# Performance work log

Measured on AMD Instinct MI355X. Metric: run time of the kernel, lower is better.

The kernel has to match this reference:

```python
import jax, jax.numpy as jnp
import numpy as np

NUM_HEADS = 4
LN_EPS = 1e-5


def setup_inputs() -> dict:
    key = jax.random.key(0)
    ks = jax.random.split(key, 5)
    C = 256
    x = jax.random.normal(ks[0], (2, C, 64, 64), dtype=jnp.float32)
    in_proj_w = jax.random.normal(ks[1], (3 * C, C), dtype=jnp.float32) * (1.0 / np.sqrt(C))
    in_proj_b = jax.random.normal(ks[2], (3 * C,), dtype=jnp.float32) * 0.02
    out_w = jax.random.normal(ks[3], (C, C), dtype=jnp.float32) * (1.0 / np.sqrt(C))
    out_b = jax.random.normal(ks[4], (C,), dtype=jnp.float32) * 0.02
    ln_g = jnp.ones((C,), dtype=jnp.float32)
    ln_b = jnp.zeros((C,), dtype=jnp.float32)
    return {"x": x, "in_proj_w": in_proj_w, "in_proj_b": in_proj_b,
            "out_w": out_w, "out_b": out_b, "ln_g": ln_g, "ln_b": ln_b}


def reference(x, in_proj_w, in_proj_b, out_w, out_b, ln_g, ln_b):
    b, c, H, W = x.shape
    S = H * W  # 4096 == max_tokens -> no pooling, no interpolation
    hd = c // NUM_HEADS
    t = x.reshape(b, c, S).transpose(0, 2, 1)  # (b, S, c)
    # fused QKV projection (in_proj_weight is [3c, c], rows = q,k,v blocks)
    qkv = t @ in_proj_w.T + in_proj_b  # (b, S, 3c)
    q, k, v = jnp.split(qkv, 3, axis=-1)
    def to_heads(a):
        return a.reshape(b, S, NUM_HEADS, hd).transpose(0, 2, 1, 3)  # (b, h, S, d)
    q = to_heads(q) * (1.0 / np.sqrt(hd))
    k = to_heads(k)
    v = to_heads(v)
    scores = jnp.einsum('bhqd,bhkd->bhqk', q, k)      # (b, h, S, S)
    probs = jax.nn.softmax(scores, axis=-1)
    attn = jnp.einsum('bhqk,bhkd->bhqd', probs, v)    # (b, h, S, d)
    attn = attn.transpose(0, 2, 1, 3).reshape(b, S, c)
    out = attn @ out_w.T + out_b                      # output projection
    # LayerNorm over channel dim
    mu = jnp.mean(out, axis=-1, keepdims=True)
    var = jnp.mean(jnp.square(out - mu), axis=-1, keepdims=True)
    out = (out - mu) * jax.lax.rsqrt(var + LN_EPS) * ln_g + ln_b
    return out.transpose(0, 2, 1).reshape(b, c, H, W)
```

## Files before the change

### kernel.cpp

```cpp
#include <hip/hip_runtime.h>
#include <cstddef>

#define S_TOK 4096
#define CDIM 256
#define NHEADS 4
#define HDIM 64
#define LSK 72
#define LDA 36
#define LDY 264
#define LOG2E 1.44269504f

typedef __attribute__((ext_vector_type(8))) short short8;
typedef __attribute__((ext_vector_type(4))) float floatx4;

__device__ inline unsigned short f2bf(float f) {
  union { float f; unsigned u; } v;
  v.f = f;
  unsigned r = v.u + 0x7fff + ((v.u >> 16) & 1);
  return (unsigned short)(r >> 16);
}
__device__ inline float bf2f(unsigned short u) {
  union { unsigned u; float f; } v;
  v.u = ((unsigned)u) << 16;
  return v.f;
}
__device__ inline unsigned pack_bf16(float a, float b) {
#if __has_builtin(__builtin_amdgcn_cvt_pk_bf16_f32)
  typedef __bf16 bf16x2 __attribute__((ext_vector_type(2)));
  union { bf16x2 v; unsigned u; } r;
  r.v = __builtin_amdgcn_cvt_pk_bf16_f32(a, b);
  return r.u;
#else
  unsigned r;
  asm("v_cvt_pk_bf16_f32 %0, %1, %2" : "=v"(r) : "v"(a), "v"(b));
  return r;
#endif
}

__device__ inline void pl32swap(unsigned& a, unsigned& b) {
  asm("v_permlane32_swap_b32 %0, %1" : "+v"(a), "+v"(b));
}
__device__ inline void pl16swap(unsigned& a, unsigned& b) {
  asm("v_permlane16_swap_b32 %0, %1" : "+v"(a), "+v"(b));
}

__global__ __launch_bounds__(256) void qkv_gemm_kernel(
    const float* __restrict__ x, const float* __restrict__ ipw,
    const float* __restrict__ ipb, unsigned short* __restrict__ q16,
    unsigned short* __restrict__ k16, unsigned short* __restrict__ vt16) {
  __shared__ __align__(16) unsigned short As[64 * LDA];
  __shared__ __align__(16) unsigned short Bs[3][64 * LDA];
  const int tid = threadIdx.x;
  const int wave = tid >> 6, lane = tid & 63;
  const int quad = lane >> 4, l16 = lane & 15;
  const int n0 = blockIdx.x * 64;
  const int tok0 = blockIdx.y * 64;
  const int b = blockIdx.z;

  const int c_l = tid >> 3, t8 = tid & 7;
  const float* gx = x + (((size_t)(b * CDIM + c_l)) << 12) + tok0 + t8 * 8;
  unsigned short* wa = &As[(t8 * 8) * LDA + c_l];

  const int rr = tid >> 2, c4 = tid & 3;
  const float* gw0 = ipw + ((size_t)(n0 + rr)) * CDIM + c4 * 8;
  unsigned short* wb0 = &Bs[0][rr * LDA + c4 * 8];

  floatx4 acc[3][4];
#pragma unroll
  for (int s = 0; s < 3; ++s)
#pragma unroll
    for (int nt = 0; nt < 4; ++nt) acc[s][nt] = (floatx4){0.f, 0.f, 0.f, 0.f};

  float4 a0 = *(const float4*)(gx);
  float4 a1 = *(const float4*)(gx + 4);
  float4 bp[3][2];
#pragma unroll
  for (int s = 0; s < 3; ++s) {
    bp[s][0] = *(const float4*)(gw0 + (size_t)s * 256 * CDIM);
    bp[s][1] = *(const float4*)(gw0 + (size_t)s * 256 * CDIM + 4);
  }

  for (int ks = 0; ks < 8; ++ks) {
    __syncthreads();
    {
      unsigned p;
      p = pack_bf16(a0.x, a0.y);
      wa[0 * LDA] = (unsigned short)p; wa[1 * LDA] = (unsigned short)(p >> 16);
      p = pack_bf16(a0.z, a0.w);
      wa[2 * LDA] = (unsigned short)p; wa[3 * LDA] = (unsigned short)(p >> 16);
      p = pack_bf16(a1.x, a1.y);
      wa[4 * LDA] = (unsigned short)p; wa[5 * LDA] = (unsigned short)(p >> 16);
      p = pack_bf16(a1.z, a1.w);
      wa[6 * LDA] = (unsigned short)p; wa[7 * LDA] = (unsigned short)(p >> 16);
    }
#pragma unroll
    for (int s = 0; s < 3; ++s) {
      uint2 u0, u1;
      u0.x = pack_bf16(bp[s][0].x, bp[s][0].y);
      u0.y = pack_bf16(bp[s][0].z, bp[s][0].w);
      u1.x = pack_bf16(bp[s][1].x, bp[s][1].y);
      u1.y = pack_bf16(bp[s][1].z, bp[s][1].w);
      unsigned short* w = wb0 + s * 64 * LDA;
      *(uint2*)w = u0;
      *(uint2*)(w + 4) = u1;
    }
    __syncthreads();
    if (ks < 7) {
      const float* gxn = gx + ((size_t)((ks + 1) * 32) << 12);
      a0 = *(const float4*)(gxn);
      a1 = *(const float4*)(gxn + 4);
#pragma unroll
      for (int s = 0; s < 3; ++s) {
        const float* g = gw0 + (size_t)s * 256 * CDIM + (ks + 1) * 32;
        bp[s][0] = *(const float4*)(g);
        bp[s][1] = *(const float4*)(g + 4);
      }
    }
    short8 af = *(const short8*)&As[(wave * 16 + l16) * LDA + quad * 8];
#pragma unroll
    for (int s = 0; s < 3; ++s)
#pragma unroll
      for (int nt = 0; nt < 4; ++nt) {
        short8 bf = *(const short8*)&Bs[s][(nt * 16 + l16) * LDA + quad * 8];
        acc[s][nt] = __builtin_amdgcn_mfma_f32_16x16x32_bf16(af, bf, acc[s][nt], 0, 0, 0);
      }
  }

  const float qsc = 0.125f * LOG2E;
#pragma unroll
  for (int nt = 0; nt < 4; ++nt) {
    int cb = n0 + nt * 16 + l16;
    int h = cb >> 6, dh = cb & 63;
    float bq = ipb[cb], bk = ipb[256 + cb], bv = ipb[512 + cb];
    size_t base = ((size_t)(b * NHEADS + h)) * S_TOK;
#pragma unroll
    for (int r = 0; r < 4; ++r) {
      int tok = tok0 + wave * 16 + quad * 4 + r;
      q16[(base + tok) * HDIM + dh] = f2bf((acc[0][nt][r] + bq) * qsc);
      k16[(base + tok) * HDIM + dh] = f2bf(acc[1][nt][r] + bk);
    }
    int tokv = tok0 + wave * 16 + quad * 4;
    uint2 u;
    u.x = pack_bf16(acc[2][nt][0] + bv, acc[2][nt][1] + bv);
    u.y = pack_bf16(acc[2][nt][2] + bv, acc[2][nt][3] + bv);
    *(uint2*)&vt16[(base * 0 + ((size_t)(b * NHEADS + h) * HDIM + dh)) * S_TOK + tokv] = u;
  }
}

__global__ __launch_bounds__(256) void attn_kernel(
    const unsigned short* __restrict__ q16,
    const unsigned short* __restrict__ k16,
    const unsigned short* __restrict__ vt16,
    unsigned short* __restrict__ op, float* __restrict__ lp) {
  __shared__ __align__(16) unsigned short Ks[2][64 * LSK];
  __shared__ __align__(16) unsigned short Vt[2][64 * LSK];

  const int tid = threadIdx.x;
  const int wave = tid >> 6;
  const int lane = tid & 63;
  const int quad = lane >> 4;
  const int l16 = lane & 15;
  const int bh = blockIdx.y;
  const int q0 = blockIdx.x * 256;
  const int split = blockIdx.z;
  const int kt0 = split * 16;

  short8 qf[4][2];
#pragma unroll
  for (int mt = 0; mt < 4; ++mt) {
    const unsigned short* qg =
        q16 + ((size_t)bh * S_TOK + q0 + wave * 64 + mt * 16 + l16) * HDIM + quad * 8;
    qf[mt][0] = *(const short8*)(qg);
    qf[mt][1] = *(const short8*)(qg + 32);
  }

  const int sr = tid >> 3, scc = tid & 7;
  const unsigned short* kg = k16 + ((size_t)bh * S_TOK + sr) * HDIM + scc * 8;
  const unsigned short* vg = vt16 + ((size_t)bh * HDIM + sr) * S_TOK + scc * 8;

  floatx4 O[4][4];
  float lsum[4] = {0.f, 0.f, 0.f, 0.f};
#pragma unroll
  for (int mt = 0; mt < 4; ++mt)
#pragma unroll
    for (int nt = 0; nt < 4; ++nt) O[mt][nt] = (floatx4){0.f, 0.f, 0.f, 0.f};

  uint4 k0r = *(const uint4*)(kg + (size_t)kt0 * 64 * HDIM);
  uint4 k1r = *(const uint4*)(kg + (size_t)kt0 * 64 * HDIM + 32 * HDIM);
  uint4 v0r = *(const uint4*)(vg + kt0 * 64);
  uint4 v1r = *(const uint4*)(vg + kt0 * 64 + (size_t)32 * S_TOK);
  {
    unsigned short* kw = &Ks[0][sr * LSK + scc * 8];
    unsigned short* vw = &Vt[0][sr * LSK + scc * 8];
    *(uint4*)kw = k0r;
    *(uint4*)(kw + 32 * LSK) = k1r;
    *(uint4*)vw = v0r;
    *(uint4*)(vw + 32 * LSK) = v1r;
  }
  __syncthreads();

  for (int t = 0; t < 16; ++t) {
    const int cur = t & 1;
    if (t < 15) {
      const unsigned short* kgn = kg + (size_t)(kt0 + t + 1) * 64 * HDIM;
      const unsigned short* vgn = vg + (kt0 + t + 1) * 64;
      k0r = *(const uint4*)(kgn);
      k1r = *(const uint4*)(kgn + 32 * HDIM);
      v0r = *(const uint4*)(vgn);
      v1r = *(const uint4*)(vgn + (size_t)32 * S_TOK);
    }
    const unsigned short* Kb = Ks[cur];
    const unsigned short* Vb = Vt[cur];

#pragma unroll
    for (int c = 0; c < 2; ++c) {
      short8 kfA0 = *(const short8*)(&Kb[((c * 2) * 16 + l16) * LSK + quad * 8]);
      short8 kfA1 = *(const short8*)(&Kb[((c * 2) * 16 + l16) * LSK + 32 + quad * 8]);
      short8 kfB0 = *(const short8*)(&Kb[((c * 2 + 1) * 16 + l16) * LSK + quad * 8]);
      short8 kfB1 = *(const short8*)(&Kb[((c * 2 + 1) * 16 + l16) * LSK + 32 + quad * 8]);
      short8 vf[4];
#pragma unroll
      for (int nt = 0; nt < 4; ++nt)
        vf[nt] = *(const short8*)(&Vb[(nt * 16 + l16) * LSK + c * 32 + quad * 8]);
#pragma unroll
      for (int mt = 0; mt < 4; ++mt) {
        floatx4 cA = (floatx4){0.f, 0.f, 0.f, 0.f};
        cA = __builtin_amdgcn_mfma_f32_16x16x32_bf16(kfA0, qf[mt][0], cA, 0, 0, 0);
        cA = __builtin_amdgcn_mfma_f32_16x16x32_bf16(kfA1, qf[mt][1], cA, 0, 0, 0);
        floatx4 cB = (floatx4){0.f, 0.f, 0.f, 0.f};
        cB = __builtin_amdgcn_mfma_f32_16x16x32_bf16(kfB0, qf[mt][0], cB, 0, 0, 0);
        cB = __builtin_amdgcn_mfma_f32_16x16x32_bf16(kfB1, qf[mt][1], cB, 0, 0, 0);
        float a0 = __builtin_amdgcn_exp2f(cA[0]);
        float a1 = __builtin_amdgcn_exp2f(cA[1]);
        float a2 = __builtin_amdgcn_exp2f(cA[2]);
        float a3 = __builtin_amdgcn_exp2f(cA[3]);
        float b0 = __builtin_amdgcn_exp2f(cB[0]);
        float b1 = __builtin_amdgcn_exp2f(cB[1]);
        float b2 = __builtin_amdgcn_exp2f(cB[2]);
        float b3 = __builtin_amdgcn_exp2f(cB[3]);
        lsum[mt] += ((a0 + a1) + (a2 + a3)) + ((b0 + b1) + (b2 + b3));
        unsigned A0 = pack_bf16(a0, a1), B0 = pack_bf16(a2, a3);
        unsigned A1 = pack_bf16(b0, b1), B1 = pack_bf16(b2, b3);
        pl32swap(A0, A1); pl16swap(A0, A1);
        pl32swap(B0, B1); pl16swap(B0, B1);
        union { uint4 u; short8 s; } pf;
        pf.u.x = A0; pf.u.y = B0; pf.u.z = A1; pf.u.w = B1;
#pragma unroll
        for (int nt = 0; nt < 4; ++nt)
          O[mt][nt] = __builtin_amdgcn_mfma_f32_16x16x32_bf16(pf.s, vf[nt], O[mt][nt], 0, 0, 0);
      }
    }

    if (t < 15) {
      unsigned short* kw = &Ks[cur ^ 1][sr * LSK + scc * 8];
      unsigned short* vw = &Vt[cur ^ 1][sr * LSK + scc * 8];
      *(uint4*)kw = k0r;
      *(uint4*)(kw + 32 * LSK) = k1r;
      *(uint4*)vw = v0r;
      *(uint4*)(vw + 32 * LSK) = v1r;
      __syncthreads();
    }
  }

  const int b = bh >> 2, h = bh & 3;
  unsigned short* op_s = op + (size_t)split * 2097152;
  float* lp_s = lp + (size_t)split * 32768;
#pragma unroll
  for (int mt = 0; mt < 4; ++mt) {
    float ls = lsum[mt];
    ls += __shfl_xor(ls, 16);
    ls += __shfl_xor(ls, 32);
    if (quad == 0)
      lp_s[bh * S_TOK + q0 + wave * 64 + mt * 16 + l16] = ls;
#pragma unroll
    for (int r = 0; r < 4; ++r) {
      int row = q0 + wave * 64 + mt * 16 + quad * 4 + r;
#pragma unroll
      for (int nt = 0; nt < 4; ++nt)
        op_s[((size_t)(b * S_TOK + row)) * CDIM + h * HDIM + nt * 16 + l16] =
            f2bf(O[mt][nt][r]);
    }
  }
}

__device__ inline uint2 merge4(const unsigned short* op, size_t off, float rinv) {
  float s0 = 0.f, s1 = 0.f, s2 = 0.f, s3 = 0.f;
#pragma unroll
  for (int sp = 0; sp < 4; ++sp) {
    uint2 u = *(const uint2*)(op + (size_t)sp * 2097152 + off);
    s0 += bf2f((unsigned short)(u.x & 0xffff));
    s1 += bf2f((unsigned short)(u.x >> 16));
    s2 += bf2f((unsigned short)(u.y & 0xffff));
    s3 += bf2f((unsigned short)(u.y >> 16));
  }
  uint2 r;
  r.x = pack_bf16(s0 * rinv, s1 * rinv);
  r.y = pack_bf16(s2 * rinv, s3 * rinv);
  return r;
}

__global__ __launch_bounds__(256) void out_ln_gemm_kernel(
    const unsigned short* __restrict__ op, const float* __restrict__ lp,
    const float* __restrict__ ow, const float* __restrict__ obias,
    const float* __restrict__ lng, const float* __restrict__ lnb,
    float* __restrict__ out) {
  __shared__ __align__(16) unsigned short As[32 * LDA];
  __shared__ __align__(16) unsigned short Bs[256 * LDA];
  __shared__ __align__(16) float ys[32 * LDY];
  __shared__ float rsum[128];
  const int tid = threadIdx.x;
  const int wave = tid >> 6, lane = tid & 63;
  const int quad = lane >> 4, l16 = lane & 15;
  const int tok0 = blockIdx.x * 32;

  if (tid < 128) {
    int t = tid >> 2, h = tid & 3;
    int bb = tok0 >> 12;
    int idx = (bb * 4 + h) * 4096 + (tok0 & 4095) + t;
    rsum[tid] =
        1.0f / (lp[idx] + lp[32768 + idx] + lp[65536 + idx] + lp[98304 + idx]);
  }
  __syncthreads();

  const int ar = tid >> 3, ac = tid & 7;
  const size_t abase = (size_t)(tok0 + ar) * CDIM + ac * 4;
  unsigned short* wAp = &As[ar * LDA + ac * 4];
  const int rr = tid >> 2, c4 = tid & 3;
  const float* gB = ow + (size_t)rr * CDIM + c4 * 8;
  unsigned short* wBp = &Bs[rr * LDA + c4 * 8];

  floatx4 acc[2][4];
#pragma unroll
  for (int mt = 0; mt < 2; ++mt)
#pragma unroll
    for (int nt = 0; nt < 4; ++nt) acc[mt][nt] = (floatx4){0.f, 0.f, 0.f, 0.f};

  uint2 ap = merge4(op, abase, rsum[(ar << 2) + (ac >> 4)]);
  float4 bpf[4][2];
#pragma unroll
  for (int i = 0; i < 4; ++i) {
    bpf[i][0] = *(const float4*)(gB + (size_t)i * 64 * CDIM);
    bpf[i][1] = *(const float4*)(gB + (size_t)i * 64 * CDIM + 4);
  }

  for (int ks = 0; ks < 8; ++ks) {
    __syncthreads();
    *(uint2*)wAp = ap;
#pragma unroll
    for (int i = 0; i < 4; ++i) {
      uint2 u0, u1;
      u0.x = pack_bf16(bpf[i][0].x, bpf[i][0].y);
      u0.y = pack_bf16(bpf[i][0].z, bpf[i][0].w);
      u1.x = pack_bf16(bpf[i][1].x, bpf[i][1].y);
      u1.y = pack_bf16(bpf[i][1].z, bpf[i][1].w);
      unsigned short* w = wBp + i * 64 * LDA;
      *(uint2*)w = u0;
      *(uint2*)(w + 4) = u1;
    }
    __syncthreads();
    if (ks < 7) {
      int off = (ks + 1) * 32;
      int ch = off + ac * 4;
      ap = merge4(op, abase + off, rsum[(ar << 2) + (ch >> 6)]);
#pragma unroll
      for (int i = 0; i < 4; ++i) {
        bpf[i][0] = *(const float4*)(gB + (size_t)i * 64 * CDIM + off);
        bpf[i][1] = *(const float4*)(gB + (size_t)i * 64 * CDIM + off + 4);
      }
    }
    short8 af[2], bf[4];
#pragma unroll
    for (int mt = 0; mt < 2; ++mt)
      af[mt] = *(const short8*)&As[(mt * 16 + l16) * LDA + quad * 8];
#pragma unroll
    for (int nt = 0; nt < 4; ++nt)
      bf[nt] = *(const short8*)&Bs[(wave * 64 + nt * 16 + l16) * LDA + quad * 8];
#pragma unroll
    for (int mt = 0; mt < 2; ++mt)
#pragma unroll
      for (int nt = 0; nt < 4; ++nt)
        acc[mt][nt] = __builtin_amdgcn_mfma_f32_16x16x32_bf16(af[mt], bf[nt], acc[mt][nt], 0, 0, 0);
  }

#pragma unroll
  for (int mt = 0; mt < 2; ++mt)
#pragma unroll
    for (int nt = 0; nt < 4; ++nt) {
      int c = wave * 64 + nt * 16 + l16;
      float bo = obias[c];
#pragma unroll
      for (int r = 0; r < 4; ++r)
        ys[(mt * 16 + quad * 4 + r) * LDY + c] = acc[mt][nt][r] + bo;
    }
  __syncthreads();

  const int gtok = tid >> 3, l8 = tid & 7;
  float sum = 0.f, ssq = 0.f;
#pragma unroll
  for (int i = 0; i < 32; ++i) {
    float v = ys[gtok * LDY + i * 8 + l8];
    sum += v;
    ssq += v * v;
  }
  sum += __shfl_xor(sum, 1); ssq += __shfl_xor(ssq, 1);
  sum += __shfl_xor(sum, 2); ssq += __shfl_xor(ssq, 2);
  sum += __shfl_xor(sum, 4); ssq += __shfl_xor(ssq, 4);
  float mu = sum * (1.f / 256.f);
  float var = ssq * (1.f / 256.f) - mu * mu;
  float rstd = rsqrtf(var + 1e-5f);
  const int b2 = tok0 >> 12;
  const int sl = (tok0 & 4095) + gtok;
#pragma unroll
  for (int i = 0; i < 32; ++i) {
    int c = i * 8 + l8;
    float v = ys[gtok * LDY + c];
    out[(((size_t)(b2 * CDIM + c)) << 12) + sl] = (v - mu) * rstd * lng[c] + lnb[c];
  }
}

extern "C" void kernel_launch(void* const* d_in, const int* in_sizes, int n_in,
                              void* d_out, int out_size, void* d_ws, size_t ws_size,
                              hipStream_t stream) {
  const float* x = (const float*)d_in[0];
  const float* ipw = (const float*)d_in[1];
  const float* ipb = (const float*)d_in[2];
  const float* ow = (const float*)d_in[3];
  const float* ob = (const float*)d_in[4];
  const float* lng = (const float*)d_in[5];
  const float* lnb = (const float*)d_in[6];
  float* out = (float*)d_out;
  unsigned short* q16 = (unsigned short*)d_ws;
  unsigned short* k16 = q16 + 2097152;
  unsigned short* vt16 = k16 + 2097152;
  unsigned short* op = vt16 + 2097152;
  float* lp = (float*)(op + 8388608);

  qkv_gemm_kernel<<<dim3(4, 64, 2), 256, 0, stream>>>(x, ipw, ipb, q16, k16, vt16);
  attn_kernel<<<dim3(16, 8, 4), 256, 0, stream>>>(q16, k16, vt16, op, lp);
  out_ln_gemm_kernel<<<256, 256, 0, stream>>>(op, lp, ow, ob, lng, lnb, out);
}
```

Before: 145.4 us.

## Pre-convert weights to bf16, add MFMA priority hints, halve output GEMM tile

A new kernel converts the QKV and output projection weights to bf16 once per call. The two GEMM kernels then load half the weight bytes and no longer pack per block. The attention kernel wraps its MFMA groups in s_setprio to favour matrix issue over the exp/pack work. The output+LayerNorm kernel now handles 16 tokens per block instead of 32, doubling the grid, at the cost of an extra launch and more redundant weight loads per token.

Measured after the change: 153.1 us. +5.3%, slower.

```diff
diff --git a/kernel.cpp b/kernel.cpp
--- a/kernel.cpp
+++ b/kernel.cpp
@@ -44,8 +44,23 @@
   asm("v_permlane16_swap_b32 %0, %1" : "+v"(a), "+v"(b));
 }
 
+__global__ __launch_bounds__(256) void convert_w_kernel(
+    const float* __restrict__ ipw, const float* __restrict__ ow,
+    unsigned short* __restrict__ wbf) {
+  int e = (blockIdx.x * 256 + threadIdx.x) * 8;
+  const float* src = (e < 196608) ? (ipw + e) : (ow + (e - 196608));
+  float4 f0 = *(const float4*)(src);
+  float4 f1 = *(const float4*)(src + 4);
+  uint4 u;
+  u.x = pack_bf16(f0.x, f0.y);
+  u.y = pack_bf16(f0.z, f0.w);
+  u.z = pack_bf16(f1.x, f1.y);
+  u.w = pack_bf16(f1.z, f1.w);
+  *(uint4*)(wbf + e) = u;
+}
+
 __global__ __launch_bounds__(256) void qkv_gemm_kernel(
-    const float* __restrict__ x, const float* __restrict__ ipw,
+    const float* __restrict__ x, const unsigned short* __restrict__ wip,
     const float* __restrict__ ipb, unsigned short* __restrict__ q16,
     unsigned short* __restrict__ k16, unsigned short* __restrict__ vt16) {
   __shared__ __align__(16) unsigned short As[64 * LDA];
@@ -62,7 +77,7 @@
   unsigned short* wa = &As[(t8 * 8) * LDA + c_l];
 
   const int rr = tid >> 2, c4 = tid & 3;
-  const float* gw0 = ipw + ((size_t)(n0 + rr)) * CDIM + c4 * 8;
+  const unsigned short* gw0 = wip + (size_t)(n0 + rr) * CDIM + c4 * 8;
   unsigned short* wb0 = &Bs[0][rr * LDA + c4 * 8];
 
   floatx4 acc[3][4];
@@ -73,12 +88,10 @@
 
   float4 a0 = *(const float4*)(gx);
   float4 a1 = *(const float4*)(gx + 4);
-  float4 bp[3][2];
-#pragma unroll
-  for (int s = 0; s < 3; ++s) {
-    bp[s][0] = *(const float4*)(gw0 + (size_t)s * 256 * CDIM);
-    bp[s][1] = *(const float4*)(gw0 + (size_t)s * 256 * CDIM + 4);
-  }
+  uint4 bp[3];
+#pragma unroll
+  for (int s = 0; s < 3; ++s)
+    bp[s] = *(const uint4*)(gw0 + (size_t)s * 256 * CDIM);
 
   for (int ks = 0; ks < 8; ++ks) {
     __syncthreads();
@@ -95,14 +108,9 @@
     }
 #pragma unroll
     for (int s = 0; s < 3; ++s) {
-      uint2 u0, u1;
-      u0.x = pack_bf16(bp[s][0].x, bp[s][0].y);
-      u0.y = pack_bf16(bp[s][0].z, bp[s][0].w);
-      u1.x = pack_bf16(bp[s][1].x, bp[s][1].y);
-      u1.y = pack_bf16(bp[s][1].z, bp[s][1].w);
       unsigned short* w = wb0 + s * 64 * LDA;
-      *(uint2*)w = u0;
-      *(uint2*)(w + 4) = u1;
+      *(uint2*)w = (uint2){bp[s].x, bp[s].y};
+      *(uint2*)(w + 4) = (uint2){bp[s].z, bp[s].w};
     }
     __syncthreads();
     if (ks < 7) {
@@ -110,11 +118,8 @@
       a0 = *(const float4*)(gxn);
       a1 = *(const float4*)(gxn + 4);
 #pragma unroll
-      for (int s = 0; s < 3; ++s) {
-        const float* g = gw0 + (size_t)s * 256 * CDIM + (ks + 1) * 32;
-        bp[s][0] = *(const float4*)(g);
-        bp[s][1] = *(const float4*)(g + 4);
-      }
+      for (int s = 0; s < 3; ++s)
+        bp[s] = *(const uint4*)(gw0 + (size_t)s * 256 * CDIM + (ks + 1) * 32);
     }
     short8 af = *(const short8*)&As[(wave * 16 + l16) * LDA + quad * 8];
 #pragma unroll
@@ -143,7 +148,7 @@
     uint2 u;
     u.x = pack_bf16(acc[2][nt][0] + bv, acc[2][nt][1] + bv);
     u.y = pack_bf16(acc[2][nt][2] + bv, acc[2][nt][3] + bv);
-    *(uint2*)&vt16[(base * 0 + ((size_t)(b * NHEADS + h) * HDIM + dh)) * S_TOK + tokv] = u;
+    *(uint2*)&vt16[((size_t)(b * NHEADS + h) * HDIM + dh) * S_TOK + tokv] = u;
   }
 }
 
@@ -224,12 +229,14 @@
         vf[nt] = *(const short8*)(&Vb[(nt * 16 + l16) * LSK + c * 32 + quad * 8]);
 #pragma unroll
       for (int mt = 0; mt < 4; ++mt) {
+        __builtin_amdgcn_s_setprio(1);
         floatx4 cA = (floatx4){0.f, 0.f, 0.f, 0.f};
         cA = __builtin_amdgcn_mfma_f32_16x16x32_bf16(kfA0, qf[mt][0], cA, 0, 0, 0);
         cA = __builtin_amdgcn_mfma_f32_16x16x32_bf16(kfA1, qf[mt][1], cA, 0, 0, 0);
         floatx4 cB = (floatx4){0.f, 0.f, 0.f, 0.f};
         cB = __builtin_amdgcn_mfma_f32_16x16x32_bf16(kfB0, qf[mt][0], cB, 0, 0, 0);
         cB = __builtin_amdgcn_mfma_f32_16x16x32_bf16(kfB1, qf[mt][1], cB, 0, 0, 0);
+        __builtin_amdgcn_s_setprio(0);
         float a0 = __builtin_amdgcn_exp2f(cA[0]);
         float a1 = __builtin_amdgcn_exp2f(cA[1]);
         float a2 = __builtin_amdgcn_exp2f(cA[2]);
@@ -245,9 +252,11 @@
         pl32swap(B0, B1); pl16swap(B0, B1);
         union { uint4 u; short8 s; } pf;
         pf.u.x = A0; pf.u.y = B0; pf.u.z = A1; pf.u.w = B1;
+        __builtin_amdgcn_s_setprio(1);
 #pragma unroll
         for (int nt = 0; nt < 4; ++nt)
           O[mt][nt] = __builtin_amdgcn_mfma_f32_16x16x32_bf16(pf.s, vf[nt], O[mt][nt], 0, 0, 0);
+        __builtin_amdgcn_s_setprio(0);
       }
     }
 
@@ -301,19 +310,19 @@
 
 __global__ __launch_bounds__(256) void out_ln_gemm_kernel(
     const unsigned short* __restrict__ op, const float* __restrict__ lp,
-    const float* __restrict__ ow, const float* __restrict__ obias,
+    const unsigned short* __restrict__ wow, const float* __restrict__ obias,
     const float* __restrict__ lng, const float* __restrict__ lnb,
     float* __restrict__ out) {
-  __shared__ __align__(16) unsigned short As[32 * LDA];
+  __shared__ __align__(16) unsigned short As[16 * LDA];
   __shared__ __align__(16) unsigned short Bs[256 * LDA];
-  __shared__ __align__(16) float ys[32 * LDY];
-  __shared__ float rsum[128];
+  __shared__ __align__(16) float ys[16 * LDY];
+  __shared__ float rsum[64];
   const int tid = threadIdx.x;
   const int wave = tid >> 6, lane = tid & 63;
   const int quad = lane >> 4, l16 = lane & 15;
-  const int tok0 = blockIdx.x * 32;
-
-  if (tid < 128) {
+  const int tok0 = blockIdx.x * 16;
+
+  if (tid < 64) {
     int t = tid >> 2, h = tid & 3;
     int bb = tok0 >> 12;
     int idx = (bb * 4 + h) * 4096 + (tok0 & 4095) + t;
@@ -326,93 +335,80 @@
   const size_t abase = (size_t)(tok0 + ar) * CDIM + ac * 4;
   unsigned short* wAp = &As[ar * LDA + ac * 4];
   const int rr = tid >> 2, c4 = tid & 3;
-  const float* gB = ow + (size_t)rr * CDIM + c4 * 8;
+  const unsigned short* gB = wow + (size_t)rr * CDIM + c4 * 8;
   unsigned short* wBp = &Bs[rr * LDA + c4 * 8];
 
-  floatx4 acc[2][4];
-#pragma unroll
-  for (int mt = 0; mt < 2; ++mt)
-#pragma unroll
-    for (int nt = 0; nt < 4; ++nt) acc[mt][nt] = (floatx4){0.f, 0.f, 0.f, 0.f};
-
-  uint2 ap = merge4(op, abase, rsum[(ar << 2) + (ac >> 4)]);
-  float4 bpf[4][2];
-#pragma unroll
-  for (int i = 0; i < 4; ++i) {
-    bpf[i][0] = *(const float4*)(gB + (size_t)i * 64 * CDIM);
-    bpf[i][1] = *(const float4*)(gB + (size_t)i * 64 * CDIM + 4);
-  }
+  floatx4 acc[4];
+#pragma unroll
+  for (int nt = 0; nt < 4; ++nt) acc[nt] = (floatx4){0.f, 0.f, 0.f, 0.f};
+
+  uint2 ap;
+  if (tid < 128) ap = merge4(op, abase, rsum[(ar << 2)]);
+  uint4 bp[4];
+#pragma unroll
+  for (int i = 0; i < 4; ++i)
+    bp[i] = *(const uint4*)(gB + (size_t)i * 64 * CDIM);
 
   for (int ks = 0; ks < 8; ++ks) {
     __syncthreads();
-    *(uint2*)wAp = ap;
+    if (tid < 128) *(uint2*)wAp = ap;
 #pragma unroll
     for (int i = 0; i < 4; ++i) {
-      uint2 u0, u1;
-      u0.x = pack_bf16(bpf[i][0].x, bpf[i][0].y);
-      u0.y = pack_bf16(bpf[i][0].z, bpf[i][0].w);
-      u1.x = pack_bf16(bpf[i][1].x, bpf[i][1].y);
-      u1.y = pack_bf16(bpf[i][1].z, bpf[i][1].w);
       unsigned short* w = wBp + i * 64 * LDA;
-      *(uint2*)w = u0;
-      *(uint2*)(w + 4) = u1;
+      *(uint2*)w = (uint2){bp[i].x, bp[i].y};
+      *(uint2*)(w + 4) = (uint2){bp[i].z, bp[i].w};
     }
     __syncthreads();
     if (ks < 7) {
       int off = (ks + 1) * 32;
-      int ch = off + ac * 4;
-      ap = merge4(op, abase + off, rsum[(ar << 2) + (ch >> 6)]);
-#pragma unroll
-      for (int i = 0; i < 4; ++i) {
-        bpf[i][0] = *(const float4*)(gB + (size_t)i * 64 * CDIM + off);
-        bpf[i][1] = *(const float4*)(gB + (size_t)i * 64 * CDIM + off + 4);
+      if (tid < 128) {
+        int ch = off + ac * 4;
+        ap = merge4(op, abase + off, rsum[(ar << 2) + (ch >> 6)]);
       }
-    }
-    short8 af[2], bf[4];
-#pragma unroll
-    for (int mt = 0; mt < 2; ++mt)
-      af[mt] = *(const short8*)&As[(mt * 16 + l16) * LDA + quad * 8];
+#pragma unroll
+      for (int i = 0; i < 4; ++i)
+        bp[i] = *(const uint4*)(gB + (size_t)i * 64 * CDIM + off);
+    }
+    short8 af = *(const short8*)&As[l16 * LDA + quad * 8];
+    short8 bf[4];
 #pragma unroll
     for (int nt = 0; nt < 4; ++nt)
       bf[nt] = *(const short8*)&Bs[(wave * 64 + nt * 16 + l16) * LDA + quad * 8];
 #pragma unroll
-    for (int mt = 0; mt < 2; ++mt)
-#pragma unroll
-      for (int nt = 0; nt < 4; ++nt)
-        acc[mt][nt] = __builtin_amdgcn_mfma_f32_16x16x32_bf16(af[mt], bf[nt], acc[mt][nt], 0, 0, 0);
-  }
-
-#pragma unroll
-  for (int mt = 0; mt < 2; ++mt)
-#pragma unroll
-    for (int nt = 0; nt < 4; ++nt) {
-      int c = wave * 64 + nt * 16 + l16;
-      float bo = obias[c];
-#pragma unroll
-      for (int r = 0; r < 4; ++r)
-        ys[(mt * 16 + quad * 4 + r) * LDY + c] = acc[mt][nt][r] + bo;
-    }
+    for (int nt = 0; nt < 4; ++nt)
+      acc[nt] = __builtin_amdgcn_mfma_f32_16x16x32_bf16(af, bf[nt], acc[nt], 0, 0, 0);
+  }
+
+#pragma unroll
+  for (int nt = 0; nt < 4; ++nt) {
+    int c = wave * 64 + nt * 16 + l16;
+    float bo = obias[c];
+#pragma unroll
+    for (int r = 0; r < 4; ++r)
+      ys[(quad * 4 + r) * LDY + c] = acc[nt][r] + bo;
+  }
   __syncthreads();
 
-  const int gtok = tid >> 3, l8 = tid & 7;
+  const int gtok = tid >> 4, lf = tid & 15;
   float sum = 0.f, ssq = 0.f;
 #pragma unroll
-  for (int i = 0; i < 32; ++i) {
-    float v = ys[gtok * LDY + i * 8 + l8];
+  for (int i = 0; i < 16; ++i) {
+    float v = ys[gtok * LDY + i * 16 + lf];
     sum += v;
     ssq += v * v;
   }
   sum += __shfl_xor(sum, 1); ssq += __shfl_xor(ssq, 1);
   sum += __shfl_xor(sum, 2); ssq += __shfl_xor(ssq, 2);
   sum += __shfl_xor(sum, 4); ssq += __shfl_xor(ssq, 4);
+  sum += __shfl_xor(sum, 8); ssq += __shfl_xor(ssq, 8);
   float mu = sum * (1.f / 256.f);
   float var = ssq * (1.f / 256.f) - mu * mu;
   float rstd = rsqrtf(var + 1e-5f);
   const int b2 = tok0 >> 12;
   const int sl = (tok0 & 4095) + gtok;
 #pragma unroll
-  for (int i = 0; i < 32; ++i) {
-    int c = i * 8 + l8;
+  for (int i = 0; i < 16; ++i) {
+    int c = i * 16 + lf;
     float v = ys[gtok * LDY + c];
     out[(((size_t)(b2 * CDIM + c)) << 12) + sl] = (v - mu) * rstd * lng[c] + lnb[c];
   }
@@ -434,8 +430,12 @@
   unsigned short* vt16 = k16 + 2097152;
   unsigned short* op = vt16 + 2097152;
   float* lp = (float*)(op + 8388608);
-
-  qkv_gemm_kernel<<<dim3(4, 64, 2), 256, 0, stream>>>(x, ipw, ipb, q16, k16, vt16);
+  unsigned short* wbf = (unsigned short*)(lp + 131072);
+  unsigned short* wip = wbf;
+  unsigned short* wow = wbf + 196608;
+
+  convert_w_kernel<<<128, 256, 0, stream>>>(ipw, ow, wbf);
+  qkv_gemm_kernel<<<dim3(4, 64, 2), 256, 0, stream>>>(x, wip, ipb, q16, k16, vt16);
   attn_kernel<<<dim3(16, 8, 4), 256, 0, stream>>>(q16, k16, vt16, op, lp);
-  out_ln_gemm_kernel<<<256, 256, 0, stream>>>(op, lp, ow, ob, lng, lnb, out);
-}
+  out_ln_gemm_kernel<<<512, 256, 0, stream>>>(op, lp, wow, ob, lng, lnb, out);
+}
```
